# Performance work log

Hardware: AMD Instinct MI355X
Metric: run time of the kernel (lower is better)

Reference implementation:

```python
import jax, jax.numpy as jnp
import numpy as np

VOCAB = 32000
D_MODEL = 512
SEQ_TABLE = 2048
EPS = 1e-5


def layer_norm(x, gamma, beta):
    mu = jnp.mean(x, axis=-1, keepdims=True)
    var = jnp.mean(jnp.square(x - mu), axis=-1, keepdims=True)
    return (x - mu) * jax.lax.rsqrt(var + EPS) * gamma + beta


def setup_inputs() -> dict:
    key = jax.random.key(0)
    ks = jax.random.split(key, 12)
    s = 0.02
    d, h, V = D_MODEL, 4 * D_MODEL, VOCAB
    return {
        "x": jax.random.randint(ks[0], (4, 2048), 0, V, dtype=jnp.int64),
        "word_emb": jax.random.normal(ks[1], (V, d), jnp.float32) * s,
        "pos_emb": jax.random.normal(ks[2], (SEQ_TABLE, d), jnp.float32) * s,
        "Wq": jax.random.normal(ks[3], (d, d), jnp.float32) * s,
        "Wk": jax.random.normal(ks[4], (d, d), jnp.float32) * s,
        "Wv": jax.random.normal(ks[5], (d, d), jnp.float32) * s,
        "g1": jnp.ones((d,), jnp.float32),
        "b1": jnp.zeros((d,), jnp.float32),
        "w_ffn1": jax.random.normal(ks[6], (h, d), jnp.float32) * s,
        "b_ffn1": jnp.zeros((h,), jnp.float32),
        "w_ffn2": jax.random.normal(ks[7], (d, h), jnp.float32) * s,
        "b_ffn2": jnp.zeros((d,), jnp.float32),
        "g2": jnp.ones((d,), jnp.float32),
        "b2": jnp.zeros((d,), jnp.float32),
        "w_vocab": jax.random.normal(ks[8], (V, d), jnp.float32) * s,
        "b_vocab": jnp.zeros((V,), jnp.float32),
    }


def reference(x, word_emb, pos_emb, Wq, Wk, Wv, g1, b1,
              w_ffn1, b_ffn1, w_ffn2, b_ffn2, g2, b2, w_vocab, b_vocab):
    B, S = x.shape
    d_k = Wq.shape[0]
    # embeddings: word + learned positional
    emb = word_emb[x] + pos_emb[jnp.arange(S)][None, :, :]  # [B,S,d]
    # single-head causal attention (torch Linear: y = x @ W.T)
    Q = emb @ Wq.T
    K = emb @ Wk.T
    V = emb @ Wv.T
    scores = jnp.einsum('bqd,bkd->bqk', Q, K) / jnp.sqrt(jnp.float32(d_k))
    causal = jnp.tril(jnp.ones((S, S), bool))
    scores = jnp.where(causal[None], scores, -jnp.inf)
    attn = jax.nn.softmax(scores, axis=-1)
    context = jnp.einsum('bqk,bkd->bqd', attn, V)
    out1 = layer_norm(emb + context, g1, b1)
    ffn = jax.nn.relu(out1 @ w_ffn1.T + b_ffn1) @ w_ffn2.T + b_ffn2
    final = layer_norm(out1 + ffn, g2, b2)
    return final @ w_vocab.T + b_vocab  # [B,S,V]
```

## Files before the change

### kernel.cpp

```cpp
#include <hip/hip_runtime.h>
#include <hip/hip_bf16.h>

typedef __bf16 bf16;
typedef __attribute__((ext_vector_type(4))) __bf16 bf16x4;
typedef __attribute__((ext_vector_type(8))) __bf16 bf16x8;
typedef __attribute__((ext_vector_type(4))) float f32x4;

__device__ inline void gload_lds16(const bf16* g, bf16* l) {
    __builtin_amdgcn_global_load_lds(
        (const __attribute__((address_space(1))) void*)g,
        (__attribute__((address_space(3))) void*)l, 16, 0, 0);
}

struct CvtArgs {
    const float* src[6];
    bf16* dst[6];
    long n4[6];
    float scale[6];
};
__global__ void embed_cvt(CvtArgs a, const int* __restrict__ x,
                          const float* __restrict__ we, const float* __restrict__ pe,
                          float* __restrict__ emb_f, bf16* __restrict__ emb_b) {
    int b = blockIdx.x;
    int tid = threadIdx.x;
    if (b < 4096) {
        int row = b * 2 + (tid >> 7);
        int c = tid & 127;
        int tok = x[row];
        int s = row & 2047;
        float4 w = ((const float4*)we)[(long)tok * 128 + c];
        float4 p = ((const float4*)pe)[(long)s * 128 + c];
        float4 e = { w.x + p.x, w.y + p.y, w.z + p.z, w.w + p.w };
        ((float4*)emb_f)[(long)row * 128 + c] = e;
        bf16x4 eb = { (bf16)e.x, (bf16)e.y, (bf16)e.z, (bf16)e.w };
        ((bf16x4*)emb_b)[(long)row * 128 + c] = eb;
    } else {
        int bb = b - 4096;
        int j  = bb >> 8;
        int bx = bb & 255;
        const float* __restrict__ src = a.src[j];
        bf16* __restrict__ dst = a.dst[j];
        long n4 = a.n4[j];
        float sc = a.scale[j];
        long i = (long)bx * 256 + tid;
        long stride = 256 * 256;
        for (; i < n4; i += stride) {
            float4 v = ((const float4*)src)[i];
            bf16x4 o = { (bf16)(v.x * sc), (bf16)(v.y * sc), (bf16)(v.z * sc), (bf16)(v.w * sc) };
            ((bf16x4*)dst)[i] = o;
        }
    }
}

template<bool WF32, int C3, bool RBIAS>
__global__ void ln_kernel(const float* __restrict__ a, const float* __restrict__ b,
                          const float* __restrict__ c, const float* __restrict__ rb,
                          const float* __restrict__ g, const float* __restrict__ bb,
                          float* __restrict__ of, bf16* __restrict__ ob) {
    int row = blockIdx.x;
    int t   = threadIdx.x;
    float4 xa = ((const float4*)a)[(long)row * 128 + t];
    float4 xb = ((const float4*)b)[(long)row * 128 + t];
    float4 xv = { xa.x + xb.x, xa.y + xb.y, xa.z + xb.z, xa.w + xb.w };
    if (C3 == 1) {
        int r = row & 2047;
        #pragma unroll
        for (int k = 1; k <= 3; k++) {
            if (r >= k * 512) {
                float4 xc = ((const float4*)(c + (long)(k - 1) * 8192 * 512))[(long)row * 128 + t];
                xv.x += xc.x; xv.y += xc.y; xv.z += xc.z; xv.w += xc.w;
            }
        }
    } else if (C3 == 2) {
        float4 xc = ((const float4*)c)[(long)row * 128 + t];
        xv.x += xc.x; xv.y += xc.y; xv.z += xc.z; xv.w += xc.w;
    }
    if (RBIAS) {
        float4 rv = ((const float4*)rb)[t];
        xv.x += rv.x; xv.y += rv.y; xv.z += rv.z; xv.w += rv.w;
    }
    float s  = xv.x + xv.y + xv.z + xv.w;
    float sq = xv.x * xv.x + xv.y * xv.y + xv.z * xv.z + xv.w * xv.w;
    #pragma unroll
    for (int o = 32; o > 0; o >>= 1) {
        s  += __shfl_xor(s, o);
        sq += __shfl_xor(sq, o);
    }
    __shared__ float rs[2], rq[2];
    int wid = t >> 6;
    if ((t & 63) == 0) { rs[wid] = s; rq[wid] = sq; }
    __syncthreads();
    s = rs[0] + rs[1]; sq = rq[0] + rq[1];
    float mu   = s * (1.0f / 512.0f);
    float var  = sq * (1.0f / 512.0f) - mu * mu;
    float rstd = rsqrtf(var + 1e-5f);
    float4 gv = ((const float4*)g)[t];
    float4 bv = ((const float4*)bb)[t];
    float4 y = { (xv.x - mu) * rstd * gv.x + bv.x,
                 (xv.y - mu) * rstd * gv.y + bv.y,
                 (xv.z - mu) * rstd * gv.z + bv.z,
                 (xv.w - mu) * rstd * gv.w + bv.w };
    if (WF32) ((float4*)of)[(long)row * 128 + t] = y;
    bf16x4 yb = { (bf16)y.x, (bf16)y.y, (bf16)y.z, (bf16)y.w };
    ((bf16x4*)ob)[(long)row * 128 + t] = yb;
}

__global__ void softmax_causal(const bf16* __restrict__ sc, bf16* __restrict__ pr) {
    int row = blockIdx.x;
    int z = row >> 11, q = row & 2047;
    const bf16* srow = sc + ((long)z * 2048 + q) * 2048;
    bf16*       prow = pr + ((long)z * 2048 + q) * 2048;
    int t = threadIdx.x;
    float v[8];
    int c0 = t * 8;
    if (t <= (q >> 3)) {
        bf16x8 vb = *(const bf16x8*)&srow[c0];
        #pragma unroll
        for (int j = 0; j < 8; j++) v[j] = (float)vb[j];
    } else {
        #pragma unroll
        for (int j = 0; j < 8; j++) v[j] = -1e30f;
    }
    float mx = -1e30f;
    #pragma unroll
    for (int j = 0; j < 8; j++) {
        if (c0 + j > q) v[j] = -1e30f;
        mx = fmaxf(mx, v[j]);
    }
    int lane = t & 63, wid = t >> 6;
    #pragma unroll
    for (int o = 32; o > 0; o >>= 1) mx = fmaxf(mx, __shfl_xor(mx, o));
    __shared__ float redm[4], reds[4];
    if (lane == 0) redm[wid] = mx;
    __syncthreads();
    mx = fmaxf(fmaxf(redm[0], redm[1]), fmaxf(redm[2], redm[3]));
    float p[8]; float sum = 0.f;
    #pragma unroll
    for (int j = 0; j < 8; j++) {
        p[j] = (c0 + j <= q) ? __expf(v[j] - mx) : 0.f;
        sum += p[j];
    }
    #pragma unroll
    for (int o = 32; o > 0; o >>= 1) sum += __shfl_xor(sum, o);
    if (lane == 0) reds[wid] = sum;
    __syncthreads();
    sum = reds[0] + reds[1] + reds[2] + reds[3];
    float inv = 1.0f / sum;
    int wlim = ((q >> 7) + 1) * 128;
    if (c0 < wlim) {
        bf16x8 o;
        #pragma unroll
        for (int j = 0; j < 8; j++) o[j] = (bf16)(p[j] * inv);
        *(bf16x8*)&prow[c0] = o;
    }
}

enum { EPI_F32 = 0, EPI_BF16 = 1, EPI_VT = 2, EPI_BIAS_RELU_BF16 = 3, EPI_BIAS_F32 = 4,
       EPI_QKV = 5, EPI_BIAS_F32_NT = 6 };
enum { ZB_BATCH = 0, ZB_PV = 1 };

template<int EPI, bool CAUSAL_SKIP, bool CAUSAL_K, bool XCD, int ZMODE>
__global__ __launch_bounds__(256)
void gemm_bt(const bf16* __restrict__ A, const bf16* __restrict__ B,
             float* __restrict__ Cf, bf16* __restrict__ Cb,
             const float* __restrict__ bias, float scale,
             int M, int N, int K, int Krow, long sA, long sB, long sC) {
    int br, bc;
    if (XCD) {
        int nwg = gridDim.x * gridDim.y;
        int lin = blockIdx.y * gridDim.x + blockIdx.x;
        lin = (lin & 7) * (nwg >> 3) + (lin >> 3);
        br = lin / gridDim.x; bc = lin - br * gridDim.x;
    } else { br = blockIdx.y; bc = blockIdx.x; }
    int z = blockIdx.z;
    int Kext = K;
    if (ZMODE == ZB_BATCH) {
        A += (long)z * sA; B += (long)z * sB; Cf += (long)z * sC; Cb += (long)z * sC;
    } else if (ZMODE == ZB_PV) {
        int batch = z >> 2, chunk = z & 3;
        A += (long)batch * sA; B += (long)batch * sB;
        Cf += (long)chunk * (8192L * 512) + (long)batch * sC;
        int keff = min(K, (br + 1) * 128);
        int lo = chunk * 512;
        if (keff <= lo) return;
        A += lo; B += lo;
        Kext = min(keff, lo + 512) - lo;
    }
    if (CAUSAL_SKIP && bc > br) return;
    if (CAUSAL_K) Kext = min(Kext, (br + 1) * 128);
    __shared__ bf16 As[128 * 64];
    __shared__ bf16 Bs[128 * 64];
    int tid = threadIdx.x;
    int lane = tid & 63, wid = tid >> 6;
    int wm = (wid >> 1) * 64, wn = (wid & 1) * 64;
    f32x4 acc[4][4] = {};
    int rowA0 = br * 128, colB0 = bc * 128;
    int rsub = lane >> 3;
    int csub = ((lane & 7) ^ rsub) * 8;
    int rdsw = (lane & 7) * 8;
    for (int kt = 0; kt < Kext; kt += 64) {
        const bf16* Ag = A + (long)rowA0 * Krow + kt;
        const bf16* Bg = B + (long)colB0 * Krow + kt;
        #pragma unroll
        for (int i = 0; i < 4; i++) {
            int seg = wid * 4 + i;
            int r = seg * 8 + rsub;
            gload_lds16(&Ag[(long)r * Krow + csub], &As[seg * 512]);
            gload_lds16(&Bg[(long)r * Krow + csub], &Bs[seg * 512]);
        }
        __syncthreads();
        #pragma unroll
        for (int kk = 0; kk < 2; kk++) {
            bf16x8 af[4], bfr[4];
            int ko = (kk * 32 + (lane >> 4) * 8) ^ rdsw;
            #pragma unroll
            for (int m = 0; m < 4; m++) af[m]  = *(const bf16x8*)&As[(wm + m * 16 + (lane & 15)) * 64 + ko];
            #pragma unroll
            for (int n = 0; n < 4; n++) bfr[n] = *(const bf16x8*)&Bs[(wn + n * 16 + (lane & 15)) * 64 + ko];
            #pragma unroll
            for (int m = 0; m < 4; m++)
                #pragma unroll
                for (int n = 0; n < 4; n++)
                    acc[m][n] = __builtin_amdgcn_mfma_f32_16x16x32_bf16(af[m], bfr[n], acc[m][n], 0, 0, 0);
        }
        __syncthreads();
    }
    #pragma unroll
    for (int m = 0; m < 4; m++) {
        #pragma unroll
        for (int n = 0; n < 4; n++) {
            #pragma unroll
            for (int j = 0; j < 4; j++) {
                int row = rowA0 + wm + m * 16 + (lane >> 4) * 4 + j;
                int col = colB0 + wn + n * 16 + (lane & 15);
                float v = acc[m][n][j];
                if (EPI == EPI_F32) {
                    Cf[(long)row * N + col] = v;
                } else if (EPI == EPI_BF16) {
                    Cb[(long)row * N + col] = (bf16)(v * scale);
                } else if (EPI == EPI_VT) {
                    int b = row >> 11, k = row & 2047;
                    Cb[((long)b * 512 + col) * 2048 + k] = (bf16)v;
                } else if (EPI == EPI_BIAS_RELU_BF16) {
                    float y = fmaxf(v + bias[col], 0.0f);
                    Cb[(long)row * N + col] = (bf16)y;
                } else if (EPI == EPI_BIAS_F32) {
                    Cf[(long)row * N + col] = v + bias[col];
                }
            }
        }
    }
}

template<int EPI, bool XCD, bool CSKIP, int BANDW, int NT>
__global__ __launch_bounds__(512)
void gemm256(const bf16* __restrict__ A, const bf16* __restrict__ B,
             float* __restrict__ Cf, bf16* __restrict__ Cb,
             const float* __restrict__ bias, int N, int K,
             long sA, long sB, long sC) {
    int br, bc;
    if (XCD) {
        int nwg = gridDim.x * gridDim.y;
        int lin = blockIdx.y * gridDim.x + blockIdx.x;
        lin = (lin & 7) * (nwg >> 3) + (lin >> 3);
        if (BANDW > 0) {
            int per = BANDW * gridDim.y;
            int band = lin / per, w2 = lin - band * per;
            br = w2 / BANDW; bc = band * BANDW + (w2 - br * BANDW);
        } else {
            br = lin / gridDim.x; bc = lin - br * gridDim.x;
        }
    } else { br = blockIdx.y; bc = blockIdx.x; }
    if (CSKIP && bc > br) return;
    int z = blockIdx.z;
    A  += (long)z * sA;
    B  += (long)z * sB;
    Cf += (long)z * sC;
    __shared__ bf16 lds[2][2][256 * 64];
    int tid = threadIdx.x;
    int lane = tid & 63, wid = tid >> 6;
    int wm2 = wid >> 2, wn4 = wid & 3;
    long rowA0 = (long)br * 256, colB0 = (long)bc * 256;
    int rsub = lane >> 3;
    int csw  = ((lane & 7) ^ rsub) * 8;
    int l15 = lane & 15;
    int rdxor = (lane & 7) << 3;
    int kbase = (lane >> 4) * 8;
    const bf16* Abase = A + rowA0 * K;
    const bf16* Bbase = B + colB0 * K;
    f32x4 acc[8][4] = {};

    auto stage = [&](int t) {
        int buf = t & 1;
        const bf16* Ag = Abase + t * 64;
        const bf16* Bg = Bbase + t * 64;
        #pragma unroll
        for (int i = 0; i < 4; i++) {
            int seg = wid * 4 + i;
            long r = seg * 8 + rsub;
            gload_lds16(&Ag[r * K + csw], &lds[buf][0][seg * 512]);
        }
        #pragma unroll
        for (int i = 0; i < 4; i++) {
            int seg = wid * 4 + i;
            long r = seg * 8 + rsub;
            gload_lds16(&Bg[r * K + csw], &lds[buf][1][seg * 512]);
        }
    };

    stage(0);
    stage(1);

    for (int t = 0; t < NT; t++) {
        int buf = t & 1;
        if (t == NT - 1) asm volatile("s_waitcnt vmcnt(0)" ::: "memory");
        else             asm volatile("s_waitcnt vmcnt(8)" ::: "memory");
        __builtin_amdgcn_s_barrier();
        const bf16* As = lds[buf][0];
        const bf16* Bs = lds[buf][1];
        bf16x8 bfr[2][4], af[2][4];
        #pragma unroll
        for (int kk = 0; kk < 2; kk++)
            #pragma unroll
            for (int n = 0; n < 4; n++) {
                int r = wn4 * 64 + n * 16 + l15;
                bfr[kk][n] = *(const bf16x8*)&Bs[r * 64 + ((kk * 32 + kbase) ^ rdxor)];
            }
        #pragma unroll
        for (int kk = 0; kk < 2; kk++)
            #pragma unroll
            for (int m = 0; m < 4; m++) {
                int r = wm2 * 128 + m * 16 + l15;
                af[kk][m] = *(const bf16x8*)&As[r * 64 + ((kk * 32 + kbase) ^ rdxor)];
            }
        __builtin_amdgcn_s_setprio(1);
        #pragma unroll
        for (int kk = 0; kk < 2; kk++)
            #pragma unroll
            for (int m = 0; m < 4; m++)
                #pragma unroll
                for (int n = 0; n < 4; n++)
                    acc[m][n] = __builtin_amdgcn_mfma_f32_16x16x32_bf16(af[kk][m], bfr[kk][n], acc[m][n], 0, 0, 0);
        __builtin_amdgcn_s_setprio(0);
        #pragma unroll
        for (int kk = 0; kk < 2; kk++)
            #pragma unroll
            for (int m = 0; m < 4; m++) {
                int r = wm2 * 128 + 64 + m * 16 + l15;
                af[kk][m] = *(const bf16x8*)&As[r * 64 + ((kk * 32 + kbase) ^ rdxor)];
            }
        asm volatile("s_waitcnt lgkmcnt(0)" ::: "memory");
        __builtin_amdgcn_sched_barrier(0);
        __builtin_amdgcn_s_barrier();
        if (t + 2 < NT) stage(t + 2);
        __builtin_amdgcn_s_setprio(1);
        #pragma unroll
        for (int kk = 0; kk < 2; kk++)
            #pragma unroll
            for (int m = 0; m < 4; m++)
                #pragma unroll
                for (int n = 0; n < 4; n++)
                    acc[4 + m][n] = __builtin_amdgcn_mfma_f32_16x16x32_bf16(af[kk][m], bfr[kk][n], acc[4 + m][n], 0, 0, 0);
        __builtin_amdgcn_s_setprio(0);
    }

    if constexpr (EPI == EPI_QKV) {
        int region = (int)(colB0 >> 9);
        if (region < 2) {
            bf16* dst = Cb + (long)region * (8192L * 512);
            int cb = ((int)colB0 & 511) + wn4 * 64;
            #pragma unroll
            for (int m = 0; m < 8; m++)
                #pragma unroll
                for (int n = 0; n < 4; n++)
                    #pragma unroll
                    for (int j = 0; j < 4; j++) {
                        long row = rowA0 + wm2 * 128 + m * 16 + (lane >> 4) * 4 + j;
                        int c = cb + n * 16 + l15;
                        dst[row * 512 + c] = (bf16)acc[m][n][j];
                    }
        } else {
            bf16* vtb = Cb + 2L * 8192 * 512;
            int cb = ((int)colB0 - 1024) + wn4 * 64;
            #pragma unroll
            for (int m = 0; m < 8; m++)
                #pragma unroll
                for (int n = 0; n < 4; n++) {
                    long k0 = rowA0 + wm2 * 128 + m * 16 + (lane >> 4) * 4;
                    long b = k0 >> 11, k = k0 & 2047;
                    int c = cb + n * 16 + l15;
                    bf16x4 pk = { (bf16)acc[m][n][0], (bf16)acc[m][n][1],
                                  (bf16)acc[m][n][2], (bf16)acc[m][n][3] };
                    *(bf16x4*)&vtb[(b * 512 + c) * 2048 + k] = pk;
                }
        }
    } else {
        #pragma unroll
        for (int m = 0; m < 8; m++) {
            #pragma unroll
            for (int n = 0; n < 4; n++) {
                #pragma unroll
                for (int j = 0; j < 4; j++) {
                    long row = rowA0 + wm2 * 128 + m * 16 + (lane >> 4) * 4 + j;
                    long col = colB0 + wn4 * 64 + n * 16 + l15;
                    float v = acc[m][n][j];
                    if (EPI == EPI_BIAS_F32) {
                        Cf[row * N + col] = v + bias[col];
                    } else if (EPI == EPI_BIAS_F32_NT) {
                        __builtin_nontemporal_store(v + bias[col], &Cf[row * N + col]);
                    } else if (EPI == EPI_BIAS_RELU_BF16) {
                        Cb[row * N + col] = (bf16)fmaxf(v + bias[col], 0.0f);
                    } else if (EPI == EPI_F32) {
                        Cf[row * N + col] = v;
                    }
                }
            }
        }
    }
}

template<int BANDB>
__global__ __launch_bounds__(256)
void gemm128v(const bf16* __restrict__ A, const bf16* __restrict__ B,
              float* __restrict__ C, const float* __restrict__ bias,
              int N, int K) {
    const int NBR = 64;
    const int NT  = 8;
    int nwg = gridDim.x;
    int lin = blockIdx.x;
    lin = (lin & 7) * (nwg >> 3) + (lin >> 3);
    int per = BANDB * NBR;
    int band = lin / per, w2 = lin - band * per;
    int br = w2 / BANDB, bc = band * BANDB + (w2 - br * BANDB);

    __shared__ bf16 lds[2][2][128 * 64];
    int tid = threadIdx.x;
    int lane = tid & 63, wid = tid >> 6;
    int wm = (wid >> 1) * 64, wn = (wid & 1) * 64;
    int rsub = lane >> 3;
    int csub = ((lane & 7) ^ rsub) * 8;
    int rdsw = (lane & 7) * 8;
    long rowA0 = (long)br * 128, colB0 = (long)bc * 128;
    const bf16* Abase = A + rowA0 * K;
    const bf16* Bbase = B + colB0 * K;
    f32x4 acc[4][4] = {};

    auto stage = [&](int t) {
        int buf = t & 1;
        const bf16* Ag = Abase + t * 64;
        const bf16* Bg = Bbase + t * 64;
        #pragma unroll
        for (int i = 0; i < 4; i++) {
            int seg = wid * 4 + i;
            long r = seg * 8 + rsub;
            gload_lds16(&Ag[r * K + csub], &lds[buf][0][seg * 512]);
        }
        #pragma unroll
        for (int i = 0; i < 4; i++) {
            int seg = wid * 4 + i;
            long r = seg * 8 + rsub;
            gload_lds16(&Bg[r * K + csub], &lds[buf][1][seg * 512]);
        }
    };

    stage(0);
    stage(1);

    for (int t = 0; t < NT; t++) {
        int buf = t & 1;
        if (t == NT - 1) asm volatile("s_waitcnt vmcnt(0)" ::: "memory");
        else             asm volatile("s_waitcnt vmcnt(8)" ::: "memory");
        __builtin_amdgcn_s_barrier();
        const bf16* As = lds[buf][0];
        const bf16* Bs = lds[buf][1];
        __builtin_amdgcn_s_setprio(1);
        #pragma unroll
        for (int kk = 0; kk < 2; kk++) {
            bf16x8 af[4], bfr[4];
            int ko = (kk * 32 + (lane >> 4) * 8) ^ rdsw;
            #pragma unroll
            for (int m = 0; m < 4; m++) af[m]  = *(const bf16x8*)&As[(wm + m * 16 + (lane & 15)) * 64 + ko];
            #pragma unroll
            for (int n = 0; n < 4; n++) bfr[n] = *(const bf16x8*)&Bs[(wn + n * 16 + (lane & 15)) * 64 + ko];
            #pragma unroll
            for (int m = 0; m < 4; m++)
                #pragma unroll
                for (int n = 0; n < 4; n++)
                    acc[m][n] = __builtin_amdgcn_mfma_f32_16x16x32_bf16(af[m], bfr[n], acc[m][n], 0, 0, 0);
        }
        __builtin_amdgcn_s_setprio(0);
        asm volatile("s_waitcnt lgkmcnt(0)" ::: "memory");
        __builtin_amdgcn_sched_barrier(0);
        __builtin_amdgcn_s_barrier();
        if (t + 2 < NT) stage(t + 2);
    }

    #pragma unroll
    for (int m = 0; m < 4; m++) {
        #pragma unroll
        for (int n = 0; n < 4; n++) {
            int col = (int)colB0 + wn + n * 16 + (lane & 15);
            float bcol = bias[col];
            #pragma unroll
            for (int j = 0; j < 4; j++) {
                long row = rowA0 + wm + m * 16 + (lane >> 4) * 4 + j;
                __builtin_nontemporal_store(acc[m][n][j] + bcol, &C[row * N + col]);
            }
        }
    }
}

extern "C" void kernel_launch(void* const* d_in, const int* in_sizes, int n_in,
                              void* d_out, int out_size, void* d_ws, size_t ws_size,
                              hipStream_t stream) {
    const int*   x       = (const int*)d_in[0];
    const float* word_emb = (const float*)d_in[1];
    const float* pos_emb  = (const float*)d_in[2];
    const float* Wq = (const float*)d_in[3];
    const float* Wk = (const float*)d_in[4];
    const float* Wv = (const float*)d_in[5];
    const float* g1 = (const float*)d_in[6];
    const float* b1 = (const float*)d_in[7];
    const float* w_ffn1 = (const float*)d_in[8];
    const float* b_ffn1 = (const float*)d_in[9];
    const float* w_ffn2 = (const float*)d_in[10];
    const float* b_ffn2 = (const float*)d_in[11];
    const float* g2 = (const float*)d_in[12];
    const float* b2 = (const float*)d_in[13];
    const float* w_vocab = (const float*)d_in[14];
    const float* b_vocab = (const float*)d_in[15];
    float* out = (float*)d_out;

    char* w = (char*)d_ws;
    auto alloc = [&](size_t bytes) { char* p = w; w += (bytes + 255) & ~255ULL; return p; };
    bf16* wqb   = (bf16*)alloc(512 * 512 * 2);
    bf16* wkb   = (bf16*)alloc(512 * 512 * 2);
    bf16* wvb   = (bf16*)alloc(512 * 512 * 2);
    bf16* w1b   = (bf16*)alloc(2048 * 512 * 2);
    bf16* w2b   = (bf16*)alloc(512 * 2048 * 2);
    bf16* wvocb = (bf16*)alloc((size_t)32000 * 512 * 2);
    float* embf = (float*)alloc((size_t)8192 * 512 * 4);
    bf16* embb  = (bf16*)alloc((size_t)8192 * 512 * 2);
    bf16* qb    = (bf16*)alloc((size_t)8192 * 512 * 2);
    bf16* kb    = (bf16*)alloc((size_t)8192 * 512 * 2);
    bf16* vt    = (bf16*)alloc((size_t)8192 * 512 * 2);
    bf16* scoresb = (bf16*)alloc((size_t)4 * 2048 * 2048 * 2);
    bf16* probs = (bf16*)alloc((size_t)4 * 2048 * 2048 * 2);
    float* ctx  = (float*)alloc((size_t)8192 * 512 * 4);
    float* pv1  = (float*)alloc((size_t)8192 * 512 * 4);
    float* pv2  = (float*)alloc((size_t)8192 * 512 * 4);
    float* pv3  = (float*)alloc((size_t)8192 * 512 * 4);
    float* out1f = (float*)alloc((size_t)8192 * 512 * 4);
    float* ffn2f = (float*)alloc((size_t)8192 * 512 * 4);
    float* ffn2b = (float*)alloc((size_t)8192 * 512 * 4);
    bf16* ffn1b = scoresb;
    bf16* out1b = kb;
    bf16* finalb = embb;
    (void)pv2; (void)pv3;

    const float qscale = 0.044194173824159216f;

    CvtArgs ca;
    ca.src[0] = Wq;      ca.dst[0] = wqb;   ca.n4[0] = 512 * 512 / 4;          ca.scale[0] = qscale;
    ca.src[1] = Wk;      ca.dst[1] = wkb;   ca.n4[1] = 512 * 512 / 4;          ca.scale[1] = 1.0f;
    ca.src[2] = Wv;      ca.dst[2] = wvb;   ca.n4[2] = 512 * 512 / 4;          ca.scale[2] = 1.0f;
    ca.src[3] = w_ffn1;  ca.dst[3] = w1b;   ca.n4[3] = 2048 * 512 / 4;         ca.scale[3] = 1.0f;
    ca.src[4] = w_ffn2;  ca.dst[4] = w2b;   ca.n4[4] = 512 * 2048 / 4;         ca.scale[4] = 1.0f;
    ca.src[5] = w_vocab; ca.dst[5] = wvocb; ca.n4[5] = (long)32000 * 512 / 4;  ca.scale[5] = 1.0f;
    embed_cvt<<<5632, 256, 0, stream>>>(ca, x, word_emb, pos_emb, embf, embb);

    gemm256<EPI_QKV, true, false, 0, 8><<<dim3(6, 32, 1), 512, 0, stream>>>(
        embb, wqb, nullptr, qb, nullptr, 1536, 512, 0, 0, 0);

    gemm_bt<EPI_BF16, true, false, false, ZB_BATCH><<<dim3(16, 16, 4), 256, 0, stream>>>(
        qb, kb, nullptr, scoresb, nullptr, 1.0f, 2048, 2048, 512, 512,
        (long)2048 * 512, (long)2048 * 512, (long)2048 * 2048);

    softmax_causal<<<8192, 256, 0, stream>>>(scoresb, probs);

    gemm_bt<EPI_F32, false, false, false, ZB_PV><<<dim3(4, 16, 16), 256, 0, stream>>>(
        probs, vt, ctx, nullptr, nullptr, 1.0f, 2048, 512, 2048, 2048,
        (long)2048 * 2048, (long)512 * 2048, (long)2048 * 512);

    ln_kernel<true, 1, false><<<8192, 128, 0, stream>>>(
        embf, ctx, pv1, nullptr, g1, b1, out1f, out1b);

    gemm256<EPI_BIAS_RELU_BF16, true, false, 0, 8><<<dim3(8, 32, 1), 512, 0, stream>>>(
        out1b, w1b, nullptr, ffn1b, b_ffn1, 2048, 512, 0, 0, 0);

    gemm_bt<EPI_F32, false, false, false, ZB_BATCH><<<dim3(4, 64, 2), 256, 0, stream>>>(
        ffn1b, w2b, ffn2f, nullptr, nullptr, 1.0f, 8192, 512, 1024, 2048,
        1024, 1024, 8192L * 512);

    ln_kernel<false, 2, true><<<8192, 128, 0, stream>>>(
        out1f, ffn2f, ffn2b, b_ffn2, g2, b2, nullptr, finalb);

    gemm128v<10><<<16000, 256, 0, stream>>>(finalb, wvocb, out, b_vocab, 32000, 512);
}
```

Before: 528.4 us.

## Store embeddings, split-K partials and residuals in bf16 instead of fp32

Removes the fp32 embedding copy and turns the PV and FFN2 split-K partial outputs into bf16 buffers. The layer-norm kernels now read bf16 residuals and partials and sum them in fp32, and the second residual uses the bf16 out1 instead of an fp32 copy. This cuts global memory traffic for the intermediate tensors in these memory-bound layer-norm and epilogue stages. The cost is lower precision, since residuals and partial sums are rounded to bf16 before accumulation.

```diff
diff --git a/kernel.cpp b/kernel.cpp
--- a/kernel.cpp
+++ b/kernel.cpp
@@ -20,7 +20,7 @@
 };
 __global__ void embed_cvt(CvtArgs a, const int* __restrict__ x,
                           const float* __restrict__ we, const float* __restrict__ pe,
-                          float* __restrict__ emb_f, bf16* __restrict__ emb_b) {
+                          bf16* __restrict__ emb_b) {
     int b = blockIdx.x;
     int tid = threadIdx.x;
     if (b < 4096) {
@@ -30,9 +30,8 @@
         int s = row & 2047;
         float4 w = ((const float4*)we)[(long)tok * 128 + c];
         float4 p = ((const float4*)pe)[(long)s * 128 + c];
-        float4 e = { w.x + p.x, w.y + p.y, w.z + p.z, w.w + p.w };
-        ((float4*)emb_f)[(long)row * 128 + c] = e;
-        bf16x4 eb = { (bf16)e.x, (bf16)e.y, (bf16)e.z, (bf16)e.w };
+        bf16x4 eb = { (bf16)(w.x + p.x), (bf16)(w.y + p.y),
+                      (bf16)(w.z + p.z), (bf16)(w.w + p.w) };
         ((bf16x4*)emb_b)[(long)row * 128 + c] = eb;
     } else {
         int bb = b - 4096;
@@ -52,28 +51,32 @@
     }
 }
 
-template<bool WF32, int C3, bool RBIAS>
-__global__ void ln_kernel(const float* __restrict__ a, const float* __restrict__ b,
-                          const float* __restrict__ c, const float* __restrict__ rb,
+template<int C3, bool RBIAS>
+__global__ void ln_kernel(const bf16* __restrict__ a, const bf16* __restrict__ c,
+                          const float* __restrict__ rb,
                           const float* __restrict__ g, const float* __restrict__ bb,
-                          float* __restrict__ of, bf16* __restrict__ ob) {
+                          bf16* __restrict__ ob) {
     int row = blockIdx.x;
     int t   = threadIdx.x;
-    float4 xa = ((const float4*)a)[(long)row * 128 + t];
-    float4 xb = ((const float4*)b)[(long)row * 128 + t];
-    float4 xv = { xa.x + xb.x, xa.y + xb.y, xa.z + xb.z, xa.w + xb.w };
+    bf16x4 av = ((const bf16x4*)a)[(long)row * 128 + t];
+    float4 xv = { (float)av[0], (float)av[1], (float)av[2], (float)av[3] };
     if (C3 == 1) {
         int r = row & 2047;
         #pragma unroll
-        for (int k = 1; k <= 3; k++) {
-            if (r >= k * 512) {
-                float4 xc = ((const float4*)(c + (long)(k - 1) * 8192 * 512))[(long)row * 128 + t];
-                xv.x += xc.x; xv.y += xc.y; xv.z += xc.z; xv.w += xc.w;
+        for (int k = 0; k < 4; k++) {
+            if (k == 0 || r >= k * 512) {
+                bf16x4 cv = ((const bf16x4*)(c + (long)k * 8192 * 512))[(long)row * 128 + t];
+                xv.x += (float)cv[0]; xv.y += (float)cv[1];
+                xv.z += (float)cv[2]; xv.w += (float)cv[3];
             }
         }
     } else if (C3 == 2) {
-        float4 xc = ((const float4*)c)[(long)row * 128 + t];
-        xv.x += xc.x; xv.y += xc.y; xv.z += xc.z; xv.w += xc.w;
+        #pragma unroll
+        for (int k = 0; k < 2; k++) {
+            bf16x4 cv = ((const bf16x4*)(c + (long)k * 8192 * 512))[(long)row * 128 + t];
+            xv.x += (float)cv[0]; xv.y += (float)cv[1];
+            xv.z += (float)cv[2]; xv.w += (float)cv[3];
+        }
     }
     if (RBIAS) {
         float4 rv = ((const float4*)rb)[t];
@@ -96,12 +99,10 @@
     float rstd = rsqrtf(var + 1e-5f);
     float4 gv = ((const float4*)g)[t];
     float4 bv = ((const float4*)bb)[t];
-    float4 y = { (xv.x - mu) * rstd * gv.x + bv.x,
-                 (xv.y - mu) * rstd * gv.y + bv.y,
-                 (xv.z - mu) * rstd * gv.z + bv.z,
-                 (xv.w - mu) * rstd * gv.w + bv.w };
-    if (WF32) ((float4*)of)[(long)row * 128 + t] = y;
-    bf16x4 yb = { (bf16)y.x, (bf16)y.y, (bf16)y.z, (bf16)y.w };
+    bf16x4 yb = { (bf16)((xv.x - mu) * rstd * gv.x + bv.x),
+                  (bf16)((xv.y - mu) * rstd * gv.y + bv.y),
+                  (bf16)((xv.z - mu) * rstd * gv.z + bv.z),
+                  (bf16)((xv.w - mu) * rstd * gv.w + bv.w) };
     ((bf16x4*)ob)[(long)row * 128 + t] = yb;
 }
 
@@ -180,6 +181,7 @@
         int batch = z >> 2, chunk = z & 3;
         A += (long)batch * sA; B += (long)batch * sB;
         Cf += (long)chunk * (8192L * 512) + (long)batch * sC;
+        Cb += (long)chunk * (8192L * 512) + (long)batch * sC;
         int keff = min(K, (br + 1) * 128);
         int lo = chunk * 512;
         if (keff <= lo) return;
@@ -539,24 +541,17 @@
     bf16* w1b   = (bf16*)alloc(2048 * 512 * 2);
     bf16* w2b   = (bf16*)alloc(512 * 2048 * 2);
     bf16* wvocb = (bf16*)alloc((size_t)32000 * 512 * 2);
-    float* embf = (float*)alloc((size_t)8192 * 512 * 4);
     bf16* embb  = (bf16*)alloc((size_t)8192 * 512 * 2);
     bf16* qb    = (bf16*)alloc((size_t)8192 * 512 * 2);
     bf16* kb    = (bf16*)alloc((size_t)8192 * 512 * 2);
     bf16* vt    = (bf16*)alloc((size_t)8192 * 512 * 2);
     bf16* scoresb = (bf16*)alloc((size_t)4 * 2048 * 2048 * 2);
     bf16* probs = (bf16*)alloc((size_t)4 * 2048 * 2048 * 2);
-    float* ctx  = (float*)alloc((size_t)8192 * 512 * 4);
-    float* pv1  = (float*)alloc((size_t)8192 * 512 * 4);
-    float* pv2  = (float*)alloc((size_t)8192 * 512 * 4);
-    float* pv3  = (float*)alloc((size_t)8192 * 512 * 4);
-    float* out1f = (float*)alloc((size_t)8192 * 512 * 4);
-    float* ffn2f = (float*)alloc((size_t)8192 * 512 * 4);
-    float* ffn2b = (float*)alloc((size_t)8192 * 512 * 4);
+    bf16* pvp   = (bf16*)alloc((size_t)4 * 8192 * 512 * 2);
+    bf16* ffn2p = (bf16*)alloc((size_t)2 * 8192 * 512 * 2);
     bf16* ffn1b = scoresb;
     bf16* out1b = kb;
     bf16* finalb = embb;
-    (void)pv2; (void)pv3;
 
     const float qscale = 0.044194173824159216f;
 
@@ -567,7 +562,7 @@
     ca.src[3] = w_ffn1;  ca.dst[3] = w1b;   ca.n4[3] = 2048 * 512 / 4;         ca.scale[3] = 1.0f;
     ca.src[4] = w_ffn2;  ca.dst[4] = w2b;   ca.n4[4] = 512 * 2048 / 4;         ca.scale[4] = 1.0f;
     ca.src[5] = w_vocab; ca.dst[5] = wvocb; ca.n4[5] = (long)32000 * 512 / 4;  ca.scale[5] = 1.0f;
-    embed_cvt<<<5632, 256, 0, stream>>>(ca, x, word_emb, pos_emb, embf, embb);
+    embed_cvt<<<5632, 256, 0, stream>>>(ca, x, word_emb, pos_emb, embb);
 
     gemm256<EPI_QKV, true, false, 0, 8><<<dim3(6, 32, 1), 512, 0, stream>>>(
         embb, wqb, nullptr, qb, nullptr, 1536, 512, 0, 0, 0);
@@ -578,22 +573,22 @@
 
     softmax_causal<<<8192, 256, 0, stream>>>(scoresb, probs);
 
-    gemm_bt<EPI_F32, false, false, false, ZB_PV><<<dim3(4, 16, 16), 256, 0, stream>>>(
-        probs, vt, ctx, nullptr, nullptr, 1.0f, 2048, 512, 2048, 2048,
+    gemm_bt<EPI_BF16, false, false, false, ZB_PV><<<dim3(4, 16, 16), 256, 0, stream>>>(
+        probs, vt, nullptr, pvp, nullptr, 1.0f, 2048, 512, 2048, 2048,
         (long)2048 * 2048, (long)512 * 2048, (long)2048 * 512);
 
-    ln_kernel<true, 1, false><<<8192, 128, 0, stream>>>(
-        embf, ctx, pv1, nullptr, g1, b1, out1f, out1b);
+    ln_kernel<1, false><<<8192, 128, 0, stream>>>(
+        embb, pvp, nullptr, g1, b1, out1b);
 
     gemm256<EPI_BIAS_RELU_BF16, true, false, 0, 8><<<dim3(8, 32, 1), 512, 0, stream>>>(
         out1b, w1b, nullptr, ffn1b, b_ffn1, 2048, 512, 0, 0, 0);
 
-    gemm_bt<EPI_F32, false, false, false, ZB_BATCH><<<dim3(4, 64, 2), 256, 0, stream>>>(
-        ffn1b, w2b, ffn2f, nullptr, nullptr, 1.0f, 8192, 512, 1024, 2048,
+    gemm_bt<EPI_BF16, false, false, false, ZB_BATCH><<<dim3(4, 64, 2), 256, 0, stream>>>(
+        ffn1b, w2b, nullptr, ffn2p, nullptr, 1.0f, 8192, 512, 1024, 2048,
         1024, 1024, 8192L * 512);
 
-    ln_kernel<false, 2, true><<<8192, 128, 0, stream>>>(
-        out1f, ffn2f, ffn2b, b_ffn2, g2, b2, nullptr, finalb);
+    ln_kernel<2, true><<<8192, 128, 0, stream>>>(
+        out1b, ffn2p, b_ffn2, g2, b2, finalb);
 
     gemm128v<10><<<16000, 256, 0, stream>>>(finalb, wvocb, out, b_vocab, 32000, 512);
 }
```

New measurement: 504.1 us. 4.6% less time.
